# Optimization experiments

Hardware: AMD Instinct MI355X
Metric: run time of the kernel (lower is better)

Reference implementation:

```python
import jax, jax.numpy as jnp
import numpy as np

N, E, D = 50000, 800000, 128   # nodes, edges, input feature dim
HEADS, HC = 8, 16
H = HEADS * HC                 # 128 hidden width after concat
G, OUT = 64, 16                # graphs in batch, output classes
EPS_BN = 1e-5


def _gat_conv(x, src, dst, edge_attr, W, att_src, att_dst, We, att_edge, b):
    """PyG GATConv (concat=True, negative_slope=0.2, add_self_loops=True,
    fill_value='mean' for edge_attr, dropout inactive in eval)."""
    n = x.shape[0]
    # self-loop edge attr = per-node mean of incoming edge attrs
    ones = jnp.ones((src.shape[0], 1), x.dtype)
    deg = jax.ops.segment_sum(ones, dst, num_segments=n)
    ea_mean = jax.ops.segment_sum(edge_attr, dst, num_segments=n) / jnp.maximum(deg, 1.0)
    loop = jnp.arange(n, dtype=src.dtype)
    src_f = jnp.concatenate([src, loop])
    dst_f = jnp.concatenate([dst, loop])
    ea = jnp.concatenate([edge_attr, ea_mean])          # [E+N, 1]
    h = (x @ W).reshape(n, HEADS, HC)                   # [N, heads, hc]
    a_src = jnp.sum(h * att_src, axis=-1)               # [N, heads]
    a_dst = jnp.sum(h * att_dst, axis=-1)               # [N, heads]
    he = (ea @ We).reshape(-1, HEADS, HC)               # [E+N, heads, hc]
    a_e = jnp.sum(he * att_edge, axis=-1)               # [E+N, heads]
    alpha = jax.nn.leaky_relu(a_src[src_f] + a_dst[dst_f] + a_e, 0.2)
    # segment softmax over destination nodes
    amax = jax.ops.segment_max(alpha, dst_f, num_segments=n)
    ex = jnp.exp(alpha - amax[dst_f])
    denom = jax.ops.segment_sum(ex, dst_f, num_segments=n)
    coef = ex / (denom[dst_f] + 1e-16)                  # [E+N, heads]
    out = jax.ops.segment_sum(h[src_f] * coef[..., None], dst_f, num_segments=n)
    return out.reshape(n, H) + b


def setup_inputs() -> dict:
    key = jax.random.key(0)
    k = lambda i: jax.random.fold_in(key, i)
    nrm = lambda i, shape, s=0.1: jax.random.normal(k(i), shape, dtype=jnp.float32) * s
    inp = {
        "x": jax.random.normal(k(0), (N, D), dtype=jnp.float32),
        "edge_index": jax.random.randint(k(1), (2, E), 0, N, dtype=jnp.int32),
        "edge_weights": jax.random.normal(k(2), (E, 1), dtype=jnp.float32),
        "batch": jnp.sort(jax.random.randint(k(3), (N,), 0, G, dtype=jnp.int32)),
        "bn_gamma": jnp.ones((D,), jnp.float32),
        "bn_beta": jnp.zeros((D,), jnp.float32),
        "bn_mean": nrm(4, (D,)),
        "bn_var": jax.random.uniform(k(5), (D,), dtype=jnp.float32) + 0.5,
    }
    ci = 10
    for li, ind in [(1, D), (2, H), (3, H)]:
        inp[f"W{li}"] = nrm(ci, (ind, H)); ci += 1
        inp[f"att_src{li}"] = nrm(ci, (HEADS, HC)); ci += 1
        inp[f"att_dst{li}"] = nrm(ci, (HEADS, HC)); ci += 1
        inp[f"We{li}"] = nrm(ci, (1, H)); ci += 1
        inp[f"att_edge{li}"] = nrm(ci, (HEADS, HC)); ci += 1
        inp[f"b{li}"] = jnp.zeros((H,), jnp.float32)
    inp["Wl1"] = nrm(40, (H, 2 * HC)); inp["bl1"] = jnp.zeros((2 * HC,), jnp.float32)
    inp["Wl2"] = nrm(41, (2 * HC, OUT)); inp["bl2"] = jnp.zeros((OUT,), jnp.float32)
    return inp


def reference(x, edge_index, edge_weights, batch,
              bn_gamma, bn_beta, bn_mean, bn_var,
              W1, att_src1, att_dst1, We1, att_edge1, b1,
              W2, att_src2, att_dst2, We2, att_edge2, b2,
              W3, att_src3, att_dst3, We3, att_edge3, b3,
              Wl1, bl1, Wl2, bl2):
    src, dst = edge_index[0], edge_index[1]
    # BatchNorm (eval mode, running stats)
    h = (x - bn_mean) / jnp.sqrt(bn_var + EPS_BN) * bn_gamma + bn_beta
    h = jax.nn.relu(_gat_conv(h, src, dst, edge_weights, W1, att_src1, att_dst1, We1, att_edge1, b1))
    h = jax.nn.relu(_gat_conv(h, src, dst, edge_weights, W2, att_src2, att_dst2, We2, att_edge2, b2))
    h = _gat_conv(h, src, dst, edge_weights, W3, att_src3, att_dst3, We3, att_edge3, b3)
    g = jax.ops.segment_max(h, batch, num_segments=G)   # global max pool -> [G, H]
    g = jax.nn.relu(g @ Wl1 + bl1)
    # dropout p=0.5 is identity in eval mode
    return g @ Wl2 + bl2
```

## Files before the change

### kernel.cpp

```cpp
#include <hip/hip_runtime.h>
#include <math.h>

#define NN 50000
#define NE 800000
#define NH 8
#define HDIM 128
#define NG 64
#define PSPLIT 16
#define NB 196
#define MAXD 64

typedef __attribute__((ext_vector_type(8))) short bf16x8;
typedef __attribute__((ext_vector_type(4))) float f32x4;

static __device__ __forceinline__ float lrelu02(float x){ return x > 0.f ? x : 0.2f*x; }
static __device__ __forceinline__ unsigned short f2bf(float f){
    unsigned u = __float_as_uint(f);
    unsigned r = (u + 0x7FFFu + ((u >> 16) & 1u)) >> 16;
    return (unsigned short)r;
}
static __device__ __forceinline__ float bf2f(unsigned short h){ return __uint_as_float((unsigned)h << 16); }
static __device__ __forceinline__ float bf_lo(unsigned v){ return __uint_as_float(v << 16); }
static __device__ __forceinline__ float bf_hi(unsigned v){ return __uint_as_float(v & 0xFFFF0000u); }

__global__ void k_prep(const float* We1, const float* ae1, const float* We2, const float* ae2,
                       const float* We3, const float* ae3, float* wev,
                       const float* gam, const float* bet, const float* mean, const float* var,
                       float* sc, float* sh){
    int t = threadIdx.x;
    if (t < 128){
        float s = gam[t] * rsqrtf(var[t] + 1e-5f);
        sc[t] = s; sh[t] = bet[t] - mean[t] * s;
    } else if (t < 152){
        int q = t - 128; int l = q >> 3, hd = q & 7;
        const float* We = (l == 0) ? We1 : (l == 1) ? We2 : We3;
        const float* ae = (l == 0) ? ae1 : (l == 1) ? ae2 : ae3;
        float s = 0.f;
        for (int c = 0; c < 16; c++) s += We[hd*16+c] * ae[hd*16+c];
        wev[q] = s;
    }
}

__global__ void k_wprep(const float* W1, const float* W2, const float* W3,
                        unsigned short* Wth, unsigned short* Wtl){
    int i = blockIdx.x*256 + threadIdx.x;
    if (i >= 3*16384) return;
    int l = i >> 14, rem = i & 16383;
    int k = rem >> 7, n = rem & 127;
    const float* W = (l==0) ? W1 : (l==1) ? W2 : W3;
    float w = W[k*128 + n];
    unsigned short hi = f2bf(w);
    unsigned short lo = f2bf(w - bf2f(hi));
    Wth[l*16384 + n*128 + k] = hi;
    Wtl[l*16384 + n*128 + k] = lo;
}

__global__ void k_scatter(const int* srcp, const int* dstp, const float* ew,
                          unsigned long long* pk, int2* tmp){
    int i = blockIdx.x*256 + threadIdx.x;
    if (i >= NE) return;
    int d = dstp[i];
    float w = ew[i];
    int fx = __float2int_rn(w * 16384.f);
    unsigned long long enc = ((unsigned long long)(unsigned)fx << 32) | 1ull;
    unsigned long long old = atomicAdd(&pk[d], enc);
    unsigned rank = (unsigned)(old & 0xFFFFFFFFull);
    if (rank < MAXD) tmp[(size_t)d*MAXD + rank] = make_int2(srcp[i], __float_as_int(w));
}

__global__ void k_scan1(const unsigned long long* pk, int* bsum){
    int i = blockIdx.x*256 + threadIdx.x;
    int v = (i < NN) ? ((const int*)pk)[2*i] + 1 : 0;
    #pragma unroll
    for (int off = 32; off >= 1; off >>= 1) v += __shfl_down(v, off);
    __shared__ int ws[4];
    if ((threadIdx.x & 63) == 0) ws[threadIdx.x >> 6] = v;
    __syncthreads();
    if (threadIdx.x == 0) bsum[blockIdx.x] = ws[0] + ws[1] + ws[2] + ws[3];
}

__global__ void k_scan2(const int* bsum, int* boff){
    __shared__ int s[256];
    int t = threadIdx.x;
    int v = (t < NB) ? bsum[t] : 0;
    s[t] = v;
    __syncthreads();
    for (int off = 1; off < 256; off <<= 1){
        int u = (t >= off) ? s[t-off] : 0;
        __syncthreads();
        s[t] += u;
        __syncthreads();
    }
    boff[t] = s[t] - v;
}

__global__ void k_scan3(const unsigned long long* pk, const int* boff, int* rowptr){
    __shared__ int s[256];
    int t = threadIdx.x;
    int i = blockIdx.x*256 + t;
    int v = (i < NN) ? ((const int*)pk)[2*i] + 1 : 0;
    s[t] = v;
    __syncthreads();
    for (int off = 1; off < 256; off <<= 1){
        int u = (t >= off) ? s[t-off] : 0;
        __syncthreads();
        s[t] += u;
        __syncthreads();
    }
    if (i < NN) rowptr[i] = boff[blockIdx.x] + s[t] - v;
    if (blockIdx.x == 0 && t == 0) rowptr[NN] = NE + NN;
}

__global__ __launch_bounds__(256) void k_compact(const unsigned long long* pk, const int* rowptr,
                          const int2* tmp, int2* es){
    int wid = threadIdx.x >> 6, l = threadIdx.x & 63;
    int n = blockIdx.x*4 + wid;
    if (n >= NN) return;
    unsigned long long pv = pk[n];
    int dg = (int)(unsigned)(pv & 0xFFFFFFFFull);
    float S = (float)(int)(unsigned)(pv >> 32) * (1.f/16384.f);
    float ea = S / fmaxf((float)dg, 1.f);
    int base = rowptr[n];
    if (l < dg) es[base + l] = tmp[(size_t)n*MAXD + l];
    if (l == 63) es[base + (dg <= 63 ? dg : 63)] = make_int2(n, __float_as_int(ea));
}

__global__ __launch_bounds__(256, 3) void k_gemm(const float* A,
        const unsigned short* Wth, const unsigned short* Wtl,
        const float* sc, const float* sh,
        const float* att_s, const float* att_d,
        unsigned* Hb, float* a_src, float* a_dst, int M){
    __shared__ unsigned short Ah[64][132];
    __shared__ unsigned short Al[64][132];
    int t = threadIdx.x;
    int row0 = blockIdx.x * 64;
    int w = t >> 6, l = t & 63;
    int lr = l & 15, lg = l >> 4;

    {
        bool bn = (sc != nullptr);
        const float2* A2 = (const float2*)A;
        for (int i = 0; i < 16; i++){
            int idx2 = t + i*256;
            int r = idx2 >> 6, c2 = idx2 & 63;
            float2 v = make_float2(0.f, 0.f);
            if (row0 + r < M){
                v = A2[(size_t)(row0+r)*64 + c2];
                if (bn){
                    float2 s2 = ((const float2*)sc)[c2], h2 = ((const float2*)sh)[c2];
                    v.x = v.x*s2.x + h2.x; v.y = v.y*s2.y + h2.y;
                }
            }
            unsigned short h0 = f2bf(v.x), h1 = f2bf(v.y);
            unsigned short l0 = f2bf(v.x - bf2f(h0)), l1 = f2bf(v.y - bf2f(h1));
            ((unsigned*)&Ah[r][0])[c2] = (unsigned)h0 | ((unsigned)h1 << 16);
            ((unsigned*)&Al[r][0])[c2] = (unsigned)l0 | ((unsigned)l1 << 16);
        }
    }
    __syncthreads();

    f32x4 acc[4][2];
    #pragma unroll
    for (int m = 0; m < 4; m++){ acc[m][0] = (f32x4){0,0,0,0}; acc[m][1] = (f32x4){0,0,0,0}; }

    #pragma unroll
    for (int ks = 0; ks < 4; ks++){
        int kk = ks*32 + lg*8;
        bf16x8 bh0 = *(const bf16x8*)&Wth[((w*2+0)*16 + lr)*128 + kk];
        bf16x8 bl0 = *(const bf16x8*)&Wtl[((w*2+0)*16 + lr)*128 + kk];
        bf16x8 bh1 = *(const bf16x8*)&Wth[((w*2+1)*16 + lr)*128 + kk];
        bf16x8 bl1 = *(const bf16x8*)&Wtl[((w*2+1)*16 + lr)*128 + kk];
        #pragma unroll
        for (int m = 0; m < 4; m++){
            bf16x8 a_h = *(const bf16x8*)&Ah[m*16 + lr][kk];
            bf16x8 a_l = *(const bf16x8*)&Al[m*16 + lr][kk];
            acc[m][0] = __builtin_amdgcn_mfma_f32_16x16x32_bf16(a_h, bh0, acc[m][0], 0, 0, 0);
            acc[m][0] = __builtin_amdgcn_mfma_f32_16x16x32_bf16(a_h, bl0, acc[m][0], 0, 0, 0);
            acc[m][0] = __builtin_amdgcn_mfma_f32_16x16x32_bf16(a_l, bh0, acc[m][0], 0, 0, 0);
            acc[m][1] = __builtin_amdgcn_mfma_f32_16x16x32_bf16(a_h, bh1, acc[m][1], 0, 0, 0);
            acc[m][1] = __builtin_amdgcn_mfma_f32_16x16x32_bf16(a_h, bl1, acc[m][1], 0, 0, 0);
            acc[m][1] = __builtin_amdgcn_mfma_f32_16x16x32_bf16(a_l, bh1, acc[m][1], 0, 0, 0);
        }
    }

    float asv[2], adv[2];
    #pragma unroll
    for (int n = 0; n < 2; n++){
        asv[n] = att_s[(w*2+n)*16 + lr];
        adv[n] = att_d[(w*2+n)*16 + lr];
    }
    #pragma unroll
    for (int m = 0; m < 4; m++){
        #pragma unroll
        for (int n = 0; n < 2; n++){
            #pragma unroll
            for (int r = 0; r < 4; r++){
                float v = acc[m][n][r];
                float pv = __shfl_xor(v, 1);
                int row = row0 + m*16 + lg*4 + r;
                if (!(l & 1) && row < M){
                    unsigned d = (unsigned)f2bf(v) | ((unsigned)f2bf(pv) << 16);
                    Hb[(size_t)row*64 + w*16 + n*8 + (lr >> 1)] = d;
                }
            }
        }
    }
    #pragma unroll
    for (int m = 0; m < 4; m++){
        #pragma unroll
        for (int r = 0; r < 4; r++){
            int row = row0 + m*16 + lg*4 + r;
            #pragma unroll
            for (int n = 0; n < 2; n++){
                float ps = acc[m][n][r] * asv[n];
                float pd = acc[m][n][r] * adv[n];
                #pragma unroll
                for (int off = 1; off < 16; off <<= 1){
                    ps += __shfl_xor(ps, off);
                    pd += __shfl_xor(pd, off);
                }
                if (lr == 0 && row < M){
                    a_src[row*NH + w*2 + n] = ps;
                    a_dst[row*NH + w*2 + n] = pd;
                }
            }
        }
    }
}

__global__ __launch_bounds__(256) void k_aggr(const int* rowptr, const int2* es,
                       const float* a_src, const float* a_dst, const float* wev,
                       const unsigned* Hb, const float* bias, float* Out, int do_relu){
    int wid = threadIdx.x >> 6, lane = threadIdx.x & 63;
    int n = blockIdx.x*4 + wid;
    if (n >= NN) return;
    int r0 = rowptr[n];
    int cnt = rowptr[n+1] - r0;
    int hd = lane >> 3;
    float ad = a_dst[n*NH + hd];
    float wh = wev[hd];
    float accL0=0.f, accL1=0.f, accH0=0.f, accH1=0.f, den0=0.f, den1=0.f;
    int e = 0;
    for (; e + 8 <= cnt; e += 8){
        int2 p[8]; unsigned v[8]; float as[8];
        #pragma unroll
        for (int j = 0; j < 8; j++) p[j] = es[r0 + e + j];
        #pragma unroll
        for (int j = 0; j < 8; j++) v[j] = Hb[(size_t)p[j].x*64 + lane];
        #pragma unroll
        for (int j = 0; j < 8; j++) as[j] = a_src[p[j].x*NH + hd];
        #pragma unroll
        for (int j = 0; j < 8; j++){
            float c = __expf(lrelu02(as[j] + ad + __int_as_float(p[j].y)*wh));
            if (j & 1){ den1 += c; accL1 += c*bf_lo(v[j]); accH1 += c*bf_hi(v[j]); }
            else      { den0 += c; accL0 += c*bf_lo(v[j]); accH0 += c*bf_hi(v[j]); }
        }
    }
    for (; e < cnt; e++){
        int2 p0 = es[r0+e];
        unsigned v0 = Hb[(size_t)p0.x*64 + lane];
        float c0 = __expf(lrelu02(a_src[p0.x*NH + hd] + ad + __int_as_float(p0.y)*wh));
        den0 += c0;
        accL0 += c0*bf_lo(v0);
        accH0 += c0*bf_hi(v0);
    }
    float inv = 1.f / (den0 + den1 + 1e-16f);
    float2 bv = ((const float2*)bias)[lane];
    float o0 = (accL0 + accL1) * inv + bv.x;
    float o1 = (accH0 + accH1) * inv + bv.y;
    if (do_relu){ o0 = fmaxf(o0, 0.f); o1 = fmaxf(o1, 0.f); }
    ((float2*)Out)[(size_t)n*64 + lane] = make_float2(o0, o1);
}

static __device__ int lower_bound_batch(const int* b, int v){
    int lo = 0, hi = NN;
    while (lo < hi){
        int mid = (lo + hi) >> 1;
        if (b[mid] < v) lo = mid + 1; else hi = mid;
    }
    return lo;
}

__global__ void k_pool1(const float* A, const int* batch, float* gpart){
    int g = blockIdx.x >> 4, s = blockIdx.x & (PSPLIT-1);
    int start = lower_bound_batch(batch, g);
    int end   = lower_bound_batch(batch, g + 1);
    int nrows = end - start;
    int chunk = (nrows + PSPLIT - 1) / PSPLIT;
    int rs = start + s*chunk;
    int re = rs + chunk; if (re > end) re = end;
    int col = threadIdx.x;
    float m = -INFINITY;
    for (int r = rs; r < re; r++) m = fmaxf(m, A[(size_t)r*HDIM + col]);
    gpart[(size_t)blockIdx.x*HDIM + col] = m;
}

__global__ void k_pool2(const float* gpart, float* gp){
    int g = blockIdx.x, col = threadIdx.x;
    float m = -INFINITY;
    for (int s = 0; s < PSPLIT; s++)
        m = fmaxf(m, gpart[(size_t)(g*PSPLIT+s)*HDIM + col]);
    gp[g*HDIM + col] = m;
}

__global__ __launch_bounds__(256) void k_mlp(const float* gp, const float* Wl1, const float* bl1,
                      const float* Wl2, const float* bl2, float* out){
    __shared__ float gl[NG*HDIM];
    __shared__ float t1[NG*32];
    int t = threadIdx.x;
    for (int i = 0; i < 8; i++)
        ((float4*)gl)[t + i*256] = ((const float4*)gp)[t + i*256];
    __syncthreads();
    for (int i = 0; i < 8; i++){
        int o = t + i*256;
        int gi = o >> 5, j = o & 31;
        float s = bl1[j];
        for (int k = 0; k < 128; k++) s += gl[gi*128 + k] * Wl1[k*32 + j];
        t1[o] = fmaxf(s, 0.f);
    }
    __syncthreads();
    for (int i = 0; i < 4; i++){
        int o = t + i*256;
        int gi = o >> 4, j = o & 15;
        float s = bl2[j];
        for (int k = 0; k < 32; k++) s += t1[gi*32 + k] * Wl2[k*16 + j];
        out[o] = s;
    }
}

extern "C" void kernel_launch(void* const* d_in, const int* in_sizes, int n_in,
                              void* d_out, int out_size, void* d_ws, size_t ws_size,
                              hipStream_t stream){
    const float* x    = (const float*)d_in[0];
    const int*   ei   = (const int*)d_in[1];
    const float* ew   = (const float*)d_in[2];
    const int*   batch= (const int*)d_in[3];
    const float* bng  = (const float*)d_in[4];
    const float* bnb  = (const float*)d_in[5];
    const float* bnm  = (const float*)d_in[6];
    const float* bnv  = (const float*)d_in[7];
    const float* Wmat[3] = {(const float*)d_in[8],  (const float*)d_in[14], (const float*)d_in[20]};
    const float* asr[3]  = {(const float*)d_in[9],  (const float*)d_in[15], (const float*)d_in[21]};
    const float* adt[3]  = {(const float*)d_in[10], (const float*)d_in[16], (const float*)d_in[22]};
    const float* Wep[3]  = {(const float*)d_in[11], (const float*)d_in[17], (const float*)d_in[23]};
    const float* aep[3]  = {(const float*)d_in[12], (const float*)d_in[18], (const float*)d_in[24]};
    const float* bp[3]   = {(const float*)d_in[13], (const float*)d_in[19], (const float*)d_in[25]};
    const float* Wl1 = (const float*)d_in[26];
    const float* bl1 = (const float*)d_in[27];
    const float* Wl2 = (const float*)d_in[28];
    const float* bl2 = (const float*)d_in[29];

    char* p = (char*)d_ws;
    auto alloc = [&](size_t bytes)->char*{
        char* r = p; p += (bytes + 255) & ~(size_t)255; return r;
    };
    float*    bufA  = (float*)alloc((size_t)NN*HDIM*4);
    unsigned* Hb    = (unsigned*)alloc((size_t)NN*64*4);
    float*    a_src = (float*)alloc((size_t)NN*NH*4);
    float*    a_dst = (float*)alloc((size_t)NN*NH*4);
    unsigned long long* pk = (unsigned long long*)alloc((size_t)NN*8);
    int*      rowptr= (int*)alloc(((size_t)NN+1)*4);
    int2*     es    = (int2*)alloc((size_t)(NE+NN)*8);
    int2*     tmp   = (int2*)alloc((size_t)NN*MAXD*8);
    int*      bsum  = (int*)alloc(256*4);
    int*      boff  = (int*)alloc(256*4);
    float*    wev   = (float*)alloc(24*4);
    float*    scv   = (float*)alloc(128*4);
    float*    shv   = (float*)alloc(128*4);
    unsigned short* Wth = (unsigned short*)alloc((size_t)3*16384*2);
    unsigned short* Wtl = (unsigned short*)alloc((size_t)3*16384*2);
    float*    gpart = (float*)alloc((size_t)NG*PSPLIT*HDIM*4);
    float*    gpool = (float*)alloc((size_t)NG*HDIM*4);

    const int* srcp = ei;
    const int* dstp = ei + NE;

    hipMemsetAsync(pk, 0, (size_t)NN*8, stream);
    k_prep<<<1, 256, 0, stream>>>(Wep[0], aep[0], Wep[1], aep[1], Wep[2], aep[2], wev,
                                  bng, bnb, bnm, bnv, scv, shv);
    k_wprep<<<192, 256, 0, stream>>>(Wmat[0], Wmat[1], Wmat[2], Wth, Wtl);
    k_scatter<<<(NE+255)/256, 256, 0, stream>>>(srcp, dstp, ew, pk, tmp);
    k_scan1<<<NB, 256, 0, stream>>>(pk, bsum);
    k_scan2<<<1, 256, 0, stream>>>(bsum, boff);
    k_scan3<<<NB, 256, 0, stream>>>(pk, boff, rowptr);
    k_compact<<<(NN+3)/4, 256, 0, stream>>>(pk, rowptr, tmp, es);

    for (int l = 0; l < 3; l++){
        const float* A  = (l == 0) ? x : bufA;
        const float* sc = (l == 0) ? scv : nullptr;
        const float* sh = (l == 0) ? shv : nullptr;
        k_gemm<<<(NN+63)/64, 256, 0, stream>>>(A, Wth + l*16384, Wtl + l*16384, sc, sh,
                                               asr[l], adt[l], Hb, a_src, a_dst, NN);
        k_aggr<<<(NN+3)/4, 256, 0, stream>>>(rowptr, es, a_src, a_dst, wev + l*8,
                                             Hb, bp[l], bufA, (l < 2) ? 1 : 0);
    }
    k_pool1<<<NG*PSPLIT, 128, 0, stream>>>(bufA, batch, gpart);
    k_pool2<<<NG, 128, 0, stream>>>(gpart, gpool);
    k_mlp<<<1, 256, 0, stream>>>(gpool, Wl1, bl1, Wl2, bl2, (float*)d_out);
}
```

Baseline: 352.8 us.

## Drop CSR build; aggregate directly from padded per-node edge slab

Removes the three scan kernels and the compact kernel. The aggregation now reads a fixed-stride per-node slab of MAXD entries and takes each node's degree and edge-weight sum straight from the packed atomic counter. Each slab entry is shrunk to 4 bytes: a 16-bit source index plus the edge weight as bf16. In aggregation, each lane computes one attention coefficient per (edge, head) and shares it by wave shuffles, so lanes no longer repeat the exp. In exchange the code relies on the node count fitting in 16 bits and accepts bf16 rounding of edge weights, and the gather loop is now serialized through shuffles.

```diff
diff --git a/kernel.cpp b/kernel.cpp
--- a/kernel.cpp
+++ b/kernel.cpp
@@ -7,7 +7,6 @@
 #define HDIM 128
 #define NG 64
 #define PSPLIT 16
-#define NB 196
 #define MAXD 64
 
 typedef __attribute__((ext_vector_type(8))) short bf16x8;
@@ -56,7 +55,7 @@
 }
 
 __global__ void k_scatter(const int* srcp, const int* dstp, const float* ew,
-                          unsigned long long* pk, int2* tmp){
+                          unsigned long long* pk, unsigned* slab){
     int i = blockIdx.x*256 + threadIdx.x;
     if (i >= NE) return;
     int d = dstp[i];
@@ -65,64 +64,10 @@
     unsigned long long enc = ((unsigned long long)(unsigned)fx << 32) | 1ull;
     unsigned long long old = atomicAdd(&pk[d], enc);
     unsigned rank = (unsigned)(old & 0xFFFFFFFFull);
-    if (rank < MAXD) tmp[(size_t)d*MAXD + rank] = make_int2(srcp[i], __float_as_int(w));
-}
-
-__global__ void k_scan1(const unsigned long long* pk, int* bsum){
-    int i = blockIdx.x*256 + threadIdx.x;
-    int v = (i < NN) ? ((const int*)pk)[2*i] + 1 : 0;
-    #pragma unroll
-    for (int off = 32; off >= 1; off >>= 1) v += __shfl_down(v, off);
-    __shared__ int ws[4];
-    if ((threadIdx.x & 63) == 0) ws[threadIdx.x >> 6] = v;
-    __syncthreads();
-    if (threadIdx.x == 0) bsum[blockIdx.x] = ws[0] + ws[1] + ws[2] + ws[3];
-}
-
-__global__ void k_scan2(const int* bsum, int* boff){
-    __shared__ int s[256];
-    int t = threadIdx.x;
-    int v = (t < NB) ? bsum[t] : 0;
-    s[t] = v;
-    __syncthreads();
-    for (int off = 1; off < 256; off <<= 1){
-        int u = (t >= off) ? s[t-off] : 0;
-        __syncthreads();
-        s[t] += u;
-        __syncthreads();
-    }
-    boff[t] = s[t] - v;
-}
-
-__global__ void k_scan3(const unsigned long long* pk, const int* boff, int* rowptr){
-    __shared__ int s[256];
-    int t = threadIdx.x;
-    int i = blockIdx.x*256 + t;
-    int v = (i < NN) ? ((const int*)pk)[2*i] + 1 : 0;
-    s[t] = v;
-    __syncthreads();
-    for (int off = 1; off < 256; off <<= 1){
-        int u = (t >= off) ? s[t-off] : 0;
-        __syncthreads();
-        s[t] += u;
-        __syncthreads();
-    }
-    if (i < NN) rowptr[i] = boff[blockIdx.x] + s[t] - v;
-    if (blockIdx.x == 0 && t == 0) rowptr[NN] = NE + NN;
-}
-
-__global__ __launch_bounds__(256) void k_compact(const unsigned long long* pk, const int* rowptr,
-                          const int2* tmp, int2* es){
-    int wid = threadIdx.x >> 6, l = threadIdx.x & 63;
-    int n = blockIdx.x*4 + wid;
-    if (n >= NN) return;
-    unsigned long long pv = pk[n];
-    int dg = (int)(unsigned)(pv & 0xFFFFFFFFull);
-    float S = (float)(int)(unsigned)(pv >> 32) * (1.f/16384.f);
-    float ea = S / fmaxf((float)dg, 1.f);
-    int base = rowptr[n];
-    if (l < dg) es[base + l] = tmp[(size_t)n*MAXD + l];
-    if (l == 63) es[base + (dg <= 63 ? dg : 63)] = make_int2(n, __float_as_int(ea));
+    if (rank < MAXD){
+        unsigned ent = (unsigned)srcp[i] | ((unsigned)f2bf(w) << 16);
+        __builtin_nontemporal_store(ent, &slab[(size_t)d*MAXD + rank]);
+    }
 }
 
 __global__ __launch_bounds__(256, 3) void k_gemm(const float* A,
@@ -228,46 +173,52 @@
     }
 }
 
-__global__ __launch_bounds__(256) void k_aggr(const int* rowptr, const int2* es,
+__global__ __launch_bounds__(256) void k_aggr(const unsigned long long* pk, const unsigned* slab,
                        const float* a_src, const float* a_dst, const float* wev,
                        const unsigned* Hb, const float* bias, float* Out, int do_relu){
     int wid = threadIdx.x >> 6, lane = threadIdx.x & 63;
     int n = blockIdx.x*4 + wid;
     if (n >= NN) return;
-    int r0 = rowptr[n];
-    int cnt = rowptr[n+1] - r0;
-    int hd = lane >> 3;
-    float ad = a_dst[n*NH + hd];
-    float wh = wev[hd];
-    float accL0=0.f, accL1=0.f, accH0=0.f, accH1=0.f, den0=0.f, den1=0.f;
-    int e = 0;
-    for (; e + 8 <= cnt; e += 8){
-        int2 p[8]; unsigned v[8]; float as[8];
-        #pragma unroll
-        for (int j = 0; j < 8; j++) p[j] = es[r0 + e + j];
-        #pragma unroll
-        for (int j = 0; j < 8; j++) v[j] = Hb[(size_t)p[j].x*64 + lane];
-        #pragma unroll
-        for (int j = 0; j < 8; j++) as[j] = a_src[p[j].x*NH + hd];
-        #pragma unroll
-        for (int j = 0; j < 8; j++){
-            float c = __expf(lrelu02(as[j] + ad + __int_as_float(p[j].y)*wh));
-            if (j & 1){ den1 += c; accL1 += c*bf_lo(v[j]); accH1 += c*bf_hi(v[j]); }
-            else      { den0 += c; accL0 += c*bf_lo(v[j]); accH0 += c*bf_hi(v[j]); }
-        }
-    }
-    for (; e < cnt; e++){
-        int2 p0 = es[r0+e];
-        unsigned v0 = Hb[(size_t)p0.x*64 + lane];
-        float c0 = __expf(lrelu02(a_src[p0.x*NH + hd] + ad + __int_as_float(p0.y)*wh));
-        den0 += c0;
-        accL0 += c0*bf_lo(v0);
-        accH0 += c0*bf_hi(v0);
-    }
-    float inv = 1.f / (den0 + den1 + 1e-16f);
+    unsigned long long pv = pk[n];
+    int dgt = (int)(unsigned)(pv & 0xFFFFFFFFull);
+    int dg  = dgt < MAXD ? dgt : MAXD;
+    float ea_self = (float)(int)(unsigned)(pv >> 32) * (1.f/16384.f) / fmaxf((float)dgt, 1.f);
+    int head  = lane & 7;
+    int ohead = lane >> 3;
+    float ad = a_dst[n*NH + head];
+    float wh = wev[head];
+    int slot = lane >> 3;
+    int cnt = dg + 1;
+    float accL = 0.f, accH = 0.f, den = 0.f;
+    for (int base = 0; base < cnt; base += 8){
+        int ei = base + slot;
+        int src; float c;
+        if (ei < dg){
+            unsigned ent = slab[(size_t)n*MAXD + ei];
+            src = (int)(ent & 0xFFFFu);
+            float eaw = bf2f((unsigned short)(ent >> 16));
+            c = __expf(lrelu02(a_src[src*NH + head] + ad + eaw*wh));
+        } else if (ei == dg){
+            src = n;
+            c = __expf(lrelu02(a_src[n*NH + head] + ad + ea_self*wh));
+        } else {
+            src = n; c = 0.f;
+        }
+        int rem = cnt - base; if (rem > 8) rem = 8;
+        #pragma unroll 8
+        for (int j = 0; j < rem; j++){
+            float cj = __shfl(c,  j*8 + ohead);
+            int   sj = __shfl(src, j*8 + ohead);
+            unsigned v = Hb[(size_t)sj*64 + lane];
+            den  += cj;
+            accL += cj*bf_lo(v);
+            accH += cj*bf_hi(v);
+        }
+    }
+    float inv = 1.f / (den + 1e-16f);
     float2 bv = ((const float2*)bias)[lane];
-    float o0 = (accL0 + accL1) * inv + bv.x;
-    float o1 = (accH0 + accH1) * inv + bv.y;
+    float o0 = accL * inv + bv.x;
+    float o1 = accH * inv + bv.y;
     if (do_relu){ o0 = fmaxf(o0, 0.f); o1 = fmaxf(o1, 0.f); }
     ((float2*)Out)[(size_t)n*64 + lane] = make_float2(o0, o1);
 }
@@ -359,11 +310,7 @@
     float*    a_src = (float*)alloc((size_t)NN*NH*4);
     float*    a_dst = (float*)alloc((size_t)NN*NH*4);
     unsigned long long* pk = (unsigned long long*)alloc((size_t)NN*8);
-    int*      rowptr= (int*)alloc(((size_t)NN+1)*4);
-    int2*     es    = (int2*)alloc((size_t)(NE+NN)*8);
-    int2*     tmp   = (int2*)alloc((size_t)NN*MAXD*8);
-    int*      bsum  = (int*)alloc(256*4);
-    int*      boff  = (int*)alloc(256*4);
+    unsigned* slab  = (unsigned*)alloc((size_t)NN*MAXD*4);
     float*    wev   = (float*)alloc(24*4);
     float*    scv   = (float*)alloc(128*4);
     float*    shv   = (float*)alloc(128*4);
@@ -379,11 +326,7 @@
     k_prep<<<1, 256, 0, stream>>>(Wep[0], aep[0], Wep[1], aep[1], Wep[2], aep[2], wev,
                                   bng, bnb, bnm, bnv, scv, shv);
     k_wprep<<<192, 256, 0, stream>>>(Wmat[0], Wmat[1], Wmat[2], Wth, Wtl);
-    k_scatter<<<(NE+255)/256, 256, 0, stream>>>(srcp, dstp, ew, pk, tmp);
-    k_scan1<<<NB, 256, 0, stream>>>(pk, bsum);
-    k_scan2<<<1, 256, 0, stream>>>(bsum, boff);
-    k_scan3<<<NB, 256, 0, stream>>>(pk, boff, rowptr);
-    k_compact<<<(NN+3)/4, 256, 0, stream>>>(pk, rowptr, tmp, es);
+    k_scatter<<<(NE+255)/256, 256, 0, stream>>>(srcp, dstp, ew, pk, slab);
 
     for (int l = 0; l < 3; l++){
         const float* A  = (l == 0) ? x : bufA;
@@ -391,7 +334,7 @@
         const float* sh = (l == 0) ? shv : nullptr;
         k_gemm<<<(NN+63)/64, 256, 0, stream>>>(A, Wth + l*16384, Wtl + l*16384, sc, sh,
                                                asr[l], adt[l], Hb, a_src, a_dst, NN);
-        k_aggr<<<(NN+3)/4, 256, 0, stream>>>(rowptr, es, a_src, a_dst, wev + l*8,
+        k_aggr<<<(NN+3)/4, 256, 0, stream>>>(pk, slab, a_src, a_dst, wev + l*8,
                                              Hb, bp[l], bufA, (l < 2) ? 1 : 0);
     }
     k_pool1<<<NG*PSPLIT, 128, 0, stream>>>(bufA, batch, gpart);
```

New measurement: 410.6 us. +16.4%, slower.
